# Kernel optimization log

Measured on AMD Instinct MI355X. Metric: run time of the kernel, lower is better.

## Reference

```python
import jax, jax.numpy as jnp
import numpy as np

B, T, C, H = 4, 1024, 1024, 16
D = C // H          # head size 64
CH = 64             # chunk size (min(T,64))
NK = T // CH        # number of key chunks
TOPK = 32           # sparse_topk
SCALE = 1.0 / np.sqrt(D)


def setup_inputs() -> dict:
    key = jax.random.key(0)
    ks = jax.random.split(key, 7)
    x = jax.random.normal(ks[0], (B, T, C), dtype=jnp.float32)
    importance_scores = jax.random.normal(ks[1], (B, T, H), dtype=jnp.float32)
    temperatures = jax.random.uniform(ks[2], (B, H), dtype=jnp.float32)
    Wq = jax.random.normal(ks[3], (C, C), dtype=jnp.float32) * 0.02
    Wk = jax.random.normal(ks[4], (C, C), dtype=jnp.float32) * 0.02
    Wv = jax.random.normal(ks[5], (C, C), dtype=jnp.float32) * 0.02
    Wo = jax.random.normal(ks[6], (C, C), dtype=jnp.float32) * 0.02
    return {"x": x, "importance_scores": importance_scores,
            "temperatures": temperatures, "Wq": Wq, "Wk": Wk, "Wv": Wv, "Wo": Wo}


def reference(x, importance_scores, temperatures, Wq, Wk, Wv, Wo):
    # projections (eval mode: all dropouts are identity)
    q = jnp.nan_to_num(x @ Wq, nan=0.0, posinf=1.0, neginf=-1.0)
    q = q.reshape(B, T, H, D).transpose(0, 2, 1, 3)            # [B,H,T,D]
    k = (x @ Wk).reshape(B, T, H, D).transpose(0, 2, 1, 3)     # [B,H,T,D]
    v = (x @ Wv).reshape(B, T, H, D).transpose(0, 2, 1, 3)
    k_ch = k.reshape(B, H, NK, CH, D)                          # key chunks
    v_ch = v.reshape(B, H, NK, CH, D)

    # scores per (query, key-chunk, in-chunk-key): [B,H,T,NK,CH]
    scores = jnp.einsum('bhqd,bhkcd->bhqkc', q, k_ch) * SCALE
    temp = jnp.clip(temperatures, 0.1, 100.0)[:, :, None, None, None]
    scores = scores / temp

    # sigmoid importance gating (per query position, broadcast over keys)
    imp = jax.nn.sigmoid(importance_scores.transpose(0, 2, 1))  # [B,H,T]
    mask_weight = jax.nn.sigmoid((imp - 0.5) * 10.0)[:, :, :, None, None]
    scores = scores * mask_weight

    # per-chunk top-k filtering (keep scores >= k-th largest, zero the rest)
    top_scores = jax.lax.top_k(scores, TOPK)[0]
    thr = top_scores[..., -1:]
    scores = scores * (scores >= thr).astype(scores.dtype)

    # per-key-chunk softmax (stable, denom clamped), as in the torch loop
    m = jnp.max(scores, axis=-1, keepdims=True)
    e = jnp.exp(scores - m)
    denom = jnp.clip(jnp.sum(e, axis=-1, keepdims=True), 1e-6, None)
    p = e / denom                                               # [B,H,T,NK,CH]

    out = jnp.einsum('bhqkc,bhkcd->bhqd', p, v_ch)              # sum over chunks
    normalizer = jnp.clip(jnp.sum(p, axis=(3, 4)), 1e-6, None)  # [B,H,T]
    out = out / normalizer[..., None]
    out = jnp.nan_to_num(out, nan=0.0, posinf=1.0, neginf=-1.0)

    out = out.transpose(0, 2, 1, 3).reshape(B, T, C)
    return out @ Wo
```

## Files before the change

### kernel.cpp

```cpp
#include <hip/hip_runtime.h>
#include <stdint.h>

typedef _Float16 f16;
typedef _Float16 f16x8 __attribute__((ext_vector_type(8)));
typedef _Float16 f16x4 __attribute__((ext_vector_type(4)));
typedef float f32x4 __attribute__((ext_vector_type(4)));

#define AS1 __attribute__((address_space(1)))
#define AS3 __attribute__((address_space(3)))

#if __has_builtin(__builtin_amdgcn_exp2f)
#define EXP2(x) __builtin_amdgcn_exp2f(x)
#else
#define EXP2(x) exp2f(x)
#endif

__device__ __forceinline__ void gl_lds16(const void* g, void* l) {
  __builtin_amdgcn_global_load_lds((const AS1 uint32_t*)g, (AS3 uint32_t*)l, 16, 0, 0);
}

__device__ __forceinline__ unsigned dpp16sum_u(unsigned v) {
  v += (unsigned)__builtin_amdgcn_update_dpp(0, (int)v, 0x121, 0xf, 0xf, true);
  v += (unsigned)__builtin_amdgcn_update_dpp(0, (int)v, 0x122, 0xf, 0xf, true);
  v += (unsigned)__builtin_amdgcn_update_dpp(0, (int)v, 0x124, 0xf, 0xf, true);
  v += (unsigned)__builtin_amdgcn_update_dpp(0, (int)v, 0x128, 0xf, 0xf, true);
  return v;
}
__device__ __forceinline__ float g16sum_f(float v) {
  v += __builtin_bit_cast(float, __builtin_amdgcn_update_dpp(0, __builtin_bit_cast(int, v), 0x121, 0xf, 0xf, true));
  v += __builtin_bit_cast(float, __builtin_amdgcn_update_dpp(0, __builtin_bit_cast(int, v), 0x122, 0xf, 0xf, true));
  v += __builtin_bit_cast(float, __builtin_amdgcn_update_dpp(0, __builtin_bit_cast(int, v), 0x124, 0xf, 0xf, true));
  v += __builtin_bit_cast(float, __builtin_amdgcn_update_dpp(0, __builtin_bit_cast(int, v), 0x128, 0xf, 0xf, true));
  return v;
}

__global__ void k_prep(const float* __restrict__ x,
                       const float* __restrict__ Wq, const float* __restrict__ Wk,
                       const float* __restrict__ Wv, const float* __restrict__ Wo,
                       f16* __restrict__ xh,
                       f16* __restrict__ Wqt, f16* __restrict__ Wkt,
                       f16* __restrict__ Wvt, f16* __restrict__ Wot) {
  __shared__ __align__(16) f16 lt[64][72];
  const int t = threadIdx.x;
  if (blockIdx.z == 4) {
    int bid2 = blockIdx.y * 16 + blockIdx.x;
    #pragma unroll 4
    for (int it = 0; it < 16; ++it) {
      int i = ((bid2 * 16 + it) * 256 + t) * 4;
      float4 v = *(const float4*)(x + i);
      f16x4 o = { (f16)v.x, (f16)v.y, (f16)v.z, (f16)v.w };
      *(f16x4*)(xh + i) = o;
    }
    return;
  }
  const float* src; f16* dst;
  switch (blockIdx.z) {
    case 0: src = Wq; dst = Wqt; break;
    case 1: src = Wk; dst = Wkt; break;
    case 2: src = Wv; dst = Wvt; break;
    default: src = Wo; dst = Wot; break;
  }
  int n0 = blockIdx.x * 64, k0 = blockIdx.y * 64;
  int kk = t >> 4;
  int nn = (t & 15) * 4;
  #pragma unroll
  for (int p = 0; p < 4; ++p) {
    int k = kk + p * 16;
    float4 v = *(const float4*)(src + (size_t)(k0 + k) * 1024 + n0 + nn);
    lt[nn + 0][k] = (f16)v.x;
    lt[nn + 1][k] = (f16)v.y;
    lt[nn + 2][k] = (f16)v.z;
    lt[nn + 3][k] = (f16)v.w;
  }
  __syncthreads();
  int row = t >> 2;
  int kp = (t & 3) * 16;
  f16* d = dst + (size_t)(n0 + row) * 1024 + k0 + kp;
  *(f16x8*)d       = *(const f16x8*)&lt[row][kp];
  *(f16x8*)(d + 8) = *(const f16x8*)&lt[row][kp + 8];
}

template<int MODE, int TM>
__global__ __launch_bounds__(256, 2)
void k_gemm(const f16* __restrict__ A, const f16* __restrict__ Bt0,
            const f16* __restrict__ Bt1, const f16* __restrict__ Bt2,
            void* __restrict__ out0, void* __restrict__ out1, void* __restrict__ out2) {
  __shared__ __align__(16) f16 As[TM * 64];
  __shared__ __align__(16) f16 Bs[128 * 64];
  __shared__ __align__(16) f16 EP[(MODE == 0) ? 4 * 64 * 72 : 4];
  const int n0 = blockIdx.x * 128, m0 = blockIdx.y * TM;
  const int tid = threadIdx.x, wave = tid >> 6, lane = tid & 63;
  const int l15 = lane & 15, quad = lane >> 4;
  const int wm = (wave >> 1) * (TM / 2), wn = (wave & 1) * 64;
  constexpr int NI = TM / 32;
  constexpr int PA = TM / 32;
  const f16* Bsrc = Bt0;
  int nb = n0;
  if (MODE == 0) {
    if (n0 >= 2048)      { Bsrc = Bt2; nb = n0 - 2048; }
    else if (n0 >= 1024) { Bsrc = Bt1; nb = n0 - 1024; }
  }
  f32x4 acc[NI][4] = {};
  const int sr = lane >> 3, sg = lane & 7;
  const int gl = sg ^ sr;
  const f16* ap[PA];
  const f16* bp[4];
  #pragma unroll
  for (int p = 0; p < PA; ++p)
    ap[p] = A + (size_t)(m0 + wave * (TM / 4) + p * 8 + sr) * 1024 + gl * 8;
  #pragma unroll
  for (int p = 0; p < 4; ++p)
    bp[p] = Bsrc + (size_t)(nb + wave * 32 + p * 8 + sr) * 1024 + gl * 8;

  for (int kt = 0; kt < 16; ++kt) {
    __syncthreads();
    #pragma unroll
    for (int p = 0; p < PA; ++p) {
      gl_lds16(ap[p], &As[(wave * (TM / 4) + p * 8) * 64]);
      ap[p] += 64;
    }
    #pragma unroll
    for (int p = 0; p < 4; ++p) {
      gl_lds16(bp[p], &Bs[(wave * 32 + p * 8) * 64]);
      bp[p] += 64;
    }
    __syncthreads();
    #pragma unroll
    for (int ks = 0; ks < 2; ++ks) {
      f16x8 af[NI], bf[4];
      #pragma unroll
      for (int i = 0; i < NI; ++i) {
        int row = wm + i * 16 + l15;
        int g2 = (ks * 4 + quad) ^ (row & 7);
        af[i] = *(const f16x8*)&As[row * 64 + g2 * 8];
      }
      #pragma unroll
      for (int j = 0; j < 4; ++j) {
        int row = wn + j * 16 + l15;
        int g2 = (ks * 4 + quad) ^ (row & 7);
        bf[j] = *(const f16x8*)&Bs[row * 64 + g2 * 8];
      }
      #pragma unroll
      for (int i = 0; i < NI; ++i)
        #pragma unroll
        for (int j = 0; j < 4; ++j)
          acc[i][j] = __builtin_amdgcn_mfma_f32_16x16x32_f16(af[i], bf[j], acc[i][j], 0, 0, 0);
    }
  }

  if (MODE == 0) {
    if (n0 < 2048) {
      f16* ep = &EP[wave * 64 * 72];
      #pragma unroll
      for (int i = 0; i < NI; ++i)
        #pragma unroll
        for (int j = 0; j < 4; ++j)
          #pragma unroll
          for (int r = 0; r < 4; ++r)
            ep[(i * 16 + quad * 4 + r) * 72 + j * 16 + l15] = (f16)acc[i][j][r];
      f16* dst = (n0 < 1024) ? (f16*)out0 : (f16*)out1;
      const int hh = ((n0 + wn) & 1023) >> 6;
      const int r8 = lane >> 3, cg = lane & 7;
      #pragma unroll
      for (int it = 0; it < 8; ++it) {
        int row = it * 8 + r8;
        f16x8 vv = *(const f16x8*)&ep[row * 72 + cg * 8];
        int m = m0 + wm + row;
        int b = m >> 10, t = m & 1023;
        *(f16x8*)&dst[(size_t)((b * 16 + hh) * 1024 + t) * 64 + cg * 8] = vv;
      }
    } else {
      #pragma unroll
      for (int i = 0; i < NI; ++i)
        #pragma unroll
        for (int j = 0; j < 4; ++j) {
          int mb = m0 + wm + i * 16 + quad * 4;
          int b = mb >> 10, t = mb & 1023;
          int n = n0 + wn + j * 16 + l15;
          int nn2 = n & 1023, hh = nn2 >> 6, d = nn2 & 63;
          f16x4 vv = { (f16)acc[i][j][0], (f16)acc[i][j][1], (f16)acc[i][j][2], (f16)acc[i][j][3] };
          *(f16x4*)((f16*)out2 + ((size_t)(b * 16 + hh) * 64 + d) * 1024 + t) = vv;
        }
    }
  } else {
    #pragma unroll
    for (int i = 0; i < NI; ++i)
      #pragma unroll
      for (int j = 0; j < 4; ++j)
        #pragma unroll
        for (int r = 0; r < 4; ++r) {
          int m = m0 + wm + i * 16 + quad * 4 + r;
          int n = n0 + wn + j * 16 + l15;
          ((float*)out0)[(size_t)m * 1024 + n] = acc[i][j][r];
        }
  }
}

__global__ __launch_bounds__(256, 4)
void k_attn(const f16* __restrict__ Q16, const f16* __restrict__ K16, const f16* __restrict__ Vt16,
            const float* __restrict__ imp, const float* __restrict__ temps,
            f16* __restrict__ part0, f16* __restrict__ part1) {
  __shared__ __align__(16) f16 Qs[64 * 64];
  __shared__ __align__(16) f16 Ks[64 * 64];
  __shared__ __align__(16) f16 Vs[64 * 64];
  __shared__ __align__(16) f16 Ps[64 * 64];

  const int bid = blockIdx.x & 1023;
  const int half = blockIdx.x >> 10;
  const int b = bid >> 8, h = (bid >> 4) & 15, qt = bid & 15;
  const int bh = b * 16 + h;
  const int tid = threadIdx.x, wave = tid >> 6, lane = tid & 63;
  const int l15 = lane & 15, quad = lane >> 4;

  float sc = (0.125f * 1.44269504088896340736f) / fminf(fmaxf(temps[bh], 0.1f), 100.0f);
  float rs[4];
  #pragma unroll
  for (int r = 0; r < 4; ++r) {
    int m = wave * 16 + quad * 4 + r;
    int t = qt * 64 + m;
    float is = imp[(size_t)(b * 1024 + t) * 16 + h];
    float s1 = 1.0f / (1.0f + __expf(-is));
    float mwv = 1.0f / (1.0f + __expf(-(s1 - 0.5f) * 10.0f));
    rs[r] = sc * mwv;
  }

  const int sr = lane >> 3, sg = lane & 7;
  const int gls = sg ^ sr;
  const size_t qoff = ((size_t)bh * 1024 + qt * 64) * 64;
  gl_lds16(Q16 + qoff + (size_t)(wave * 16 + sr) * 64 + gls * 8,     &Qs[(wave * 16) * 64]);
  gl_lds16(Q16 + qoff + (size_t)(wave * 16 + 8 + sr) * 64 + gls * 8, &Qs[(wave * 16 + 8) * 64]);

  const size_t kbase = (size_t)bh * 1024 * 64;
  const size_t vbase = (size_t)bh * 64 * 1024;
  const f16* kp0 = K16 + kbase + (size_t)(half * 512 + wave * 16 + sr) * 64 + gls * 8;
  const f16* kp1 = kp0 + 8 * 64;
  const f16* vp0 = Vt16 + vbase + (size_t)(wave * 16 + sr) * 1024 + half * 512 + gls * 8;
  const f16* vp1 = vp0 + 8 * 1024;
  f16* lk0 = &Ks[(wave * 16) * 64];
  f16* lk1 = &Ks[(wave * 16 + 8) * 64];
  f16* lv0 = &Vs[(wave * 16) * 64];
  f16* lv1 = &Vs[(wave * 16 + 8) * 64];

  f32x4 oacc[4] = {};

  for (int ck = 0; ck < 8; ++ck) {
    __syncthreads();
    gl_lds16(kp0, lk0); gl_lds16(kp1, lk1);
    gl_lds16(vp0, lv0); gl_lds16(vp1, lv1);
    kp0 += 4096; kp1 += 4096; vp0 += 64; vp1 += 64;
    __syncthreads();

    f32x4 sacc[4] = {};
    #pragma unroll
    for (int ks = 0; ks < 2; ++ks) {
      int row = wave * 16 + l15;
      int g2 = (ks * 4 + quad) ^ (row & 7);
      f16x8 aq = *(const f16x8*)&Qs[row * 64 + g2 * 8];
      #pragma unroll
      for (int j = 0; j < 4; ++j) {
        int rn = j * 16 + l15;
        int gn = (ks * 4 + quad) ^ (rn & 7);
        f16x8 bk = *(const f16x8*)&Ks[rn * 64 + gn * 8];
        sacc[j] = __builtin_amdgcn_mfma_f32_16x16x32_f16(aq, bk, sacc[j], 0, 0, 0);
      }
    }

    float svc[4][4];
    unsigned key[4][4];
    #pragma unroll
    for (int j = 0; j < 4; ++j)
      #pragma unroll
      for (int r = 0; r < 4; ++r) {
        float xx = __builtin_amdgcn_fmed3f(sacc[j][r] * rs[r], -60.0f, 60.0f);
        svc[j][r] = xx;
        key[j][r] = __builtin_bit_cast(unsigned, xx + 3072.0f);
      }

    unsigned tk0 = 0x45000000u, tk1 = 0x45000000u, tk2 = 0x45000000u, tk3 = 0x45000000u;
    #pragma unroll
    for (int bit = 15; bit >= 0; --bit) {
      const unsigned bpv = 1u << (7 + bit);
      unsigned c0 = tk0 | bpv, c1 = tk1 | bpv, c2 = tk2 | bpv, c3 = tk3 | bpv;
      unsigned pk = 0;
      #pragma unroll
      for (int j = 0; j < 4; ++j) {
        pk += (key[j][0] >= c0) ? 1u : 0u;
        pk += (key[j][1] >= c1) ? 0x100u : 0u;
        pk += (key[j][2] >= c2) ? 0x10000u : 0u;
        pk += (key[j][3] >= c3) ? 0x1000000u : 0u;
      }
      pk = dpp16sum_u(pk);
      unsigned ge = ((pk | 0x80808080u) - 0x20202020u) & 0x80808080u;
      tk0 = (ge & 0x80u) ? c0 : tk0;
      tk1 = (ge & 0x8000u) ? c1 : tk1;
      tk2 = (ge & 0x800000u) ? c2 : tk2;
      tk3 = (ge & 0x80000000u) ? c3 : tk3;
    }
    const unsigned tkr0 = tk0, tkr1 = tk1, tkr2 = tk2, tkr3 = tk3;

    float e[4][4], dinv[4];
    {
      const unsigned tks[4] = { tkr0, tkr1, tkr2, tkr3 };
      #pragma unroll
      for (int r = 0; r < 4; ++r) {
        #pragma unroll
        for (int j = 0; j < 4; ++j) {
          float xv = (key[j][r] >= tks[r]) ? svc[j][r] : 0.0f;
          e[j][r] = EXP2(xv);
        }
        float d = (e[0][r] + e[1][r]) + (e[2][r] + e[3][r]);
        d = g16sum_f(d);
        dinv[r] = __builtin_amdgcn_rcpf(d);
      }
    }

    #pragma unroll
    for (int j = 0; j < 4; ++j)
      #pragma unroll
      for (int r = 0; r < 4; ++r) {
        int m = wave * 16 + quad * 4 + r;
        int c = j * 16 + l15;
        int g2 = (c >> 3) ^ (m & 7);
        Ps[m * 64 + g2 * 8 + (c & 7)] = (f16)(e[j][r] * dinv[r]);
      }

    #pragma unroll
    for (int ks = 0; ks < 2; ++ks) {
      int row = wave * 16 + l15;
      int g2 = (ks * 4 + quad) ^ (row & 7);
      f16x8 ap2 = *(const f16x8*)&Ps[row * 64 + g2 * 8];
      #pragma unroll
      for (int j = 0; j < 4; ++j) {
        int rn = j * 16 + l15;
        int gn = (ks * 4 + quad) ^ (rn & 7);
        f16x8 bv = *(const f16x8*)&Vs[rn * 64 + gn * 8];
        oacc[j] = __builtin_amdgcn_mfma_f32_16x16x32_f16(ap2, bv, oacc[j], 0, 0, 0);
      }
    }
  }

  f16* pd = half ? part1 : part0;
  #pragma unroll
  for (int j = 0; j < 4; ++j)
    #pragma unroll
    for (int r = 0; r < 4; ++r) {
      int m = wave * 16 + quad * 4 + r;
      int t = qt * 64 + m;
      int d = j * 16 + l15;
      pd[(size_t)(b * 1024 + t) * 1024 + h * 64 + d] = (f16)oacc[j][r];
    }
}

__global__ void k_combine(const f16* __restrict__ p0, f16* __restrict__ o) {
  int i = (blockIdx.x * 256 + threadIdx.x) * 8;
  f16x8 a = *(const f16x8*)(p0 + i);
  f16x8 bb = *(const f16x8*)(o + i);
  f16x8 r;
  #pragma unroll
  for (int k = 0; k < 8; ++k)
    r[k] = (f16)(((float)a[k] + (float)bb[k]) * 0.0625f);
  *(f16x8*)(o + i) = r;
}

extern "C" void kernel_launch(void* const* d_in, const int* in_sizes, int n_in,
                              void* d_out, int out_size, void* d_ws, size_t ws_size,
                              hipStream_t stream) {
  (void)in_sizes; (void)n_in; (void)out_size; (void)ws_size;
  const float* x     = (const float*)d_in[0];
  const float* imp   = (const float*)d_in[1];
  const float* temps = (const float*)d_in[2];
  const float* Wq    = (const float*)d_in[3];
  const float* Wk    = (const float*)d_in[4];
  const float* Wv    = (const float*)d_in[5];
  const float* Wo    = (const float*)d_in[6];
  float* out = (float*)d_out;

  char* w = (char*)d_ws;
  f16* xh   = (f16*)w; w += (size_t)4096 * 1024 * 2;
  f16* Wqt  = (f16*)w; w += (size_t)1024 * 1024 * 2;
  f16* Wkt  = (f16*)w; w += (size_t)1024 * 1024 * 2;
  f16* Wvt  = (f16*)w; w += (size_t)1024 * 1024 * 2;
  f16* Wot  = (f16*)w; w += (size_t)1024 * 1024 * 2;
  f16* Q16  = (f16*)w; w += (size_t)4096 * 1024 * 2;
  f16* K16  = (f16*)w; w += (size_t)4096 * 1024 * 2;
  f16* Vt16 = (f16*)w; w += (size_t)4096 * 1024 * 2;
  f16* O16  = (f16*)w; w += (size_t)4096 * 1024 * 2;

  k_prep<<<dim3(16, 16, 5), dim3(256), 0, stream>>>(x, Wq, Wk, Wv, Wo, xh, Wqt, Wkt, Wvt, Wot);
  k_gemm<0, 128><<<dim3(24, 32), dim3(256), 0, stream>>>(xh, Wqt, Wkt, Wvt,
                                                         (void*)Q16, (void*)K16, (void*)Vt16);
  k_attn<<<dim3(2048), dim3(256), 0, stream>>>(Q16, K16, Vt16, imp, temps, xh, O16);
  k_combine<<<dim3(2048), dim3(256), 0, stream>>>(xh, O16);
  k_gemm<2, 64><<<dim3(8, 64), dim3(256), 0, stream>>>(O16, Wot, nullptr, nullptr,
                                                       (void*)out, nullptr, nullptr);
}
```

Measured before the change: 269.8 us.

## Fuse partial-sum combine into output GEMM and shorten top-k radix search

Removes the separate combine kernel. The output projection GEMM now loads both attention partial buffers, adds them in registers and writes the sum to LDS, with the 1/16 normalisation folded into the Wo weights during prep. The top-k threshold bit search also drops from 16 to 13 iterations by using a smaller float bias, so the key encoding covers a narrower exponent range. The cost is that the A-operand load in that GEMM switches from direct global-to-LDS copies to register loads plus LDS stores, and the shorter search may change threshold precision.

Result: faster. 262.0 us (-2.9%).

```diff
diff --git a/kernel.cpp b/kernel.cpp
--- a/kernel.cpp
+++ b/kernel.cpp
@@ -53,12 +53,12 @@
     }
     return;
   }
-  const float* src; f16* dst;
+  const float* src; f16* dst; float scl;
   switch (blockIdx.z) {
-    case 0: src = Wq; dst = Wqt; break;
-    case 1: src = Wk; dst = Wkt; break;
-    case 2: src = Wv; dst = Wvt; break;
-    default: src = Wo; dst = Wot; break;
+    case 0: src = Wq; dst = Wqt; scl = 1.0f; break;
+    case 1: src = Wk; dst = Wkt; scl = 1.0f; break;
+    case 2: src = Wv; dst = Wvt; scl = 1.0f; break;
+    default: src = Wo; dst = Wot; scl = 0.0625f; break;
   }
   int n0 = blockIdx.x * 64, k0 = blockIdx.y * 64;
   int kk = t >> 4;
@@ -67,10 +67,10 @@
   for (int p = 0; p < 4; ++p) {
     int k = kk + p * 16;
     float4 v = *(const float4*)(src + (size_t)(k0 + k) * 1024 + n0 + nn);
-    lt[nn + 0][k] = (f16)v.x;
-    lt[nn + 1][k] = (f16)v.y;
-    lt[nn + 2][k] = (f16)v.z;
-    lt[nn + 3][k] = (f16)v.w;
+    lt[nn + 0][k] = (f16)(v.x * scl);
+    lt[nn + 1][k] = (f16)(v.y * scl);
+    lt[nn + 2][k] = (f16)(v.z * scl);
+    lt[nn + 3][k] = (f16)(v.w * scl);
   }
   __syncthreads();
   int row = t >> 2;
@@ -83,7 +83,8 @@
 template<int MODE, int TM>
 __global__ __launch_bounds__(256, 2)
 void k_gemm(const f16* __restrict__ A, const f16* __restrict__ Bt0,
-            const f16* __restrict__ Bt1, const f16* __restrict__ Bt2,
+            const f16* __restrict__ A2, const f16* __restrict__ Bt2,
+            const f16* __restrict__ Bt1,
             void* __restrict__ out0, void* __restrict__ out1, void* __restrict__ out2) {
   __shared__ __align__(16) f16 As[TM * 64];
   __shared__ __align__(16) f16 Bs[128 * 64];
@@ -104,10 +105,14 @@
   const int sr = lane >> 3, sg = lane & 7;
   const int gl = sg ^ sr;
   const f16* ap[PA];
+  const f16* ap2[PA];
   const f16* bp[4];
   #pragma unroll
-  for (int p = 0; p < PA; ++p)
-    ap[p] = A + (size_t)(m0 + wave * (TM / 4) + p * 8 + sr) * 1024 + gl * 8;
+  for (int p = 0; p < PA; ++p) {
+    size_t off = (size_t)(m0 + wave * (TM / 4) + p * 8 + sr) * 1024 + gl * 8;
+    ap[p] = A + off;
+    if (MODE == 2) ap2[p] = A2 + off;
+  }
   #pragma unroll
   for (int p = 0; p < 4; ++p)
     bp[p] = Bsrc + (size_t)(nb + wave * 32 + p * 8 + sr) * 1024 + gl * 8;
@@ -116,7 +121,14 @@
     __syncthreads();
     #pragma unroll
     for (int p = 0; p < PA; ++p) {
-      gl_lds16(ap[p], &As[(wave * (TM / 4) + p * 8) * 64]);
+      if (MODE == 2) {
+        f16x8 a0 = *(const f16x8*)ap[p];
+        f16x8 a1 = *(const f16x8*)ap2[p];
+        *(f16x8*)&As[(wave * (TM / 4) + p * 8) * 64 + lane * 8] = a0 + a1;
+        ap2[p] += 64;
+      } else {
+        gl_lds16(ap[p], &As[(wave * (TM / 4) + p * 8) * 64]);
+      }
       ap[p] += 64;
     }
     #pragma unroll
@@ -273,13 +285,13 @@
       for (int r = 0; r < 4; ++r) {
         float xx = __builtin_amdgcn_fmed3f(sacc[j][r] * rs[r], -60.0f, 60.0f);
         svc[j][r] = xx;
-        key[j][r] = __builtin_bit_cast(unsigned, xx + 3072.0f);
-      }
-
-    unsigned tk0 = 0x45000000u, tk1 = 0x45000000u, tk2 = 0x45000000u, tk3 = 0x45000000u;
-    #pragma unroll
-    for (int bit = 15; bit >= 0; --bit) {
-      const unsigned bpv = 1u << (7 + bit);
+        key[j][r] = __builtin_bit_cast(unsigned, xx + 192.0f);
+      }
+
+    unsigned tk0 = 0x43000000u, tk1 = 0x43000000u, tk2 = 0x43000000u, tk3 = 0x43000000u;
+    #pragma unroll
+    for (int bit = 12; bit >= 0; --bit) {
+      const unsigned bpv = 1u << (10 + bit);
       unsigned c0 = tk0 | bpv, c1 = tk1 | bpv, c2 = tk2 | bpv, c3 = tk3 | bpv;
       unsigned pk = 0;
       #pragma unroll
@@ -296,22 +308,19 @@
       tk2 = (ge & 0x800000u) ? c2 : tk2;
       tk3 = (ge & 0x80000000u) ? c3 : tk3;
     }
-    const unsigned tkr0 = tk0, tkr1 = tk1, tkr2 = tk2, tkr3 = tk3;
 
     float e[4][4], dinv[4];
-    {
-      const unsigned tks[4] = { tkr0, tkr1, tkr2, tkr3 };
-      #pragma unroll
-      for (int r = 0; r < 4; ++r) {
-        #pragma unroll
-        for (int j = 0; j < 4; ++j) {
-          float xv = (key[j][r] >= tks[r]) ? svc[j][r] : 0.0f;
-          e[j][r] = EXP2(xv);
-        }
-        float d = (e[0][r] + e[1][r]) + (e[2][r] + e[3][r]);
-        d = g16sum_f(d);
-        dinv[r] = __builtin_amdgcn_rcpf(d);
-      }
+    #pragma unroll
+    for (int r = 0; r < 4; ++r) {
+      const unsigned tkc = (r == 0) ? tk0 : (r == 1) ? tk1 : (r == 2) ? tk2 : tk3;
+      #pragma unroll
+      for (int j = 0; j < 4; ++j) {
+        float xv = (key[j][r] >= tkc) ? svc[j][r] : 0.0f;
+        e[j][r] = EXP2(xv);
+      }
+      float d = (e[0][r] + e[1][r]) + (e[2][r] + e[3][r]);
+      d = g16sum_f(d);
+      dinv[r] = __builtin_amdgcn_rcpf(d);
     }
 
     #pragma unroll
@@ -349,17 +358,6 @@
       int d = j * 16 + l15;
       pd[(size_t)(b * 1024 + t) * 1024 + h * 64 + d] = (f16)oacc[j][r];
     }
-}
-
-__global__ void k_combine(const f16* __restrict__ p0, f16* __restrict__ o) {
-  int i = (blockIdx.x * 256 + threadIdx.x) * 8;
-  f16x8 a = *(const f16x8*)(p0 + i);
-  f16x8 bb = *(const f16x8*)(o + i);
-  f16x8 r;
-  #pragma unroll
-  for (int k = 0; k < 8; ++k)
-    r[k] = (f16)(((float)a[k] + (float)bb[k]) * 0.0625f);
-  *(f16x8*)(o + i) = r;
 }
 
 extern "C" void kernel_launch(void* const* d_in, const int* in_sizes, int n_in,
@@ -387,10 +385,9 @@
   f16* O16  = (f16*)w; w += (size_t)4096 * 1024 * 2;
 
   k_prep<<<dim3(16, 16, 5), dim3(256), 0, stream>>>(x, Wq, Wk, Wv, Wo, xh, Wqt, Wkt, Wvt, Wot);
-  k_gemm<0, 128><<<dim3(24, 32), dim3(256), 0, stream>>>(xh, Wqt, Wkt, Wvt,
+  k_gemm<0, 128><<<dim3(24, 32), dim3(256), 0, stream>>>(xh, Wqt, nullptr, Wvt, Wkt,
                                                          (void*)Q16, (void*)K16, (void*)Vt16);
   k_attn<<<dim3(2048), dim3(256), 0, stream>>>(Q16, K16, Vt16, imp, temps, xh, O16);
-  k_combine<<<dim3(2048), dim3(256), 0, stream>>>(xh, O16);
-  k_gemm<2, 64><<<dim3(8, 64), dim3(256), 0, stream>>>(O16, Wot, nullptr, nullptr,
+  k_gemm<2, 64><<<dim3(8, 64), dim3(256), 0, stream>>>(xh, Wot, O16, nullptr, nullptr,
                                                        (void*)out, nullptr, nullptr);
 }
```
